# Performance work log

Measured on AMD Instinct MI355X. Metric: run time of the kernel, lower is better.

The kernel has to match this reference:

```python
import jax, jax.numpy as jnp
import numpy as np

NUM_ITER = 64
M_CONST = jnp.array([-1.0, 1.0], dtype=jnp.float32)      # constellation m
ALPHA   = jnp.array([0.5, 0.5], dtype=jnp.float32)       # prior alpha


def setup_inputs() -> dict:
    key = jax.random.key(0)
    k1, k2, k3 = jax.random.split(key, 3)
    B, N_RX, N_TX = 16384, 64, 32
    # channel matrix, scaled ~1/sqrt(N_rx) like a normalized MIMO channel
    Ht = jax.random.normal(k1, (B, N_RX, N_TX), dtype=jnp.float32) / jnp.sqrt(jnp.float32(N_RX))
    yt = jax.random.normal(k2, (B, N_RX), dtype=jnp.float32)
    sigmat0 = jax.random.uniform(k3, (B,), dtype=jnp.float32, minval=0.1, maxval=0.6)
    taui = jnp.ones((NUM_ITER + 1,), dtype=jnp.float32)          # taui0 = 1
    delta = jnp.full((NUM_ITER,), 0.01, dtype=jnp.float32)       # small step size for stability
    return {"yt": yt, "Ht": Ht, "sigmat0": sigmat0, "taui": taui, "delta": delta}


def _cmdnet(yt, Ht, sigmat0, taui, delta):
    m = M_CONST                      # [M]
    log_alpha = jnp.log(ALPHA)       # [M]
    sig2 = (sigmat0 ** 2)[:, None, None]          # [B,1,1]
    B, _, K = Ht.shape
    M = m.shape[0]

    # G0 = zeros broadcast to [B, K, M]
    G = jnp.zeros((B, K, M), dtype=Ht.dtype)
    tau = jnp.abs(taui[0])
    ft = jax.nn.softmax((log_alpha + G) * tau, axis=-1)   # [B,K,M]
    xt = jnp.sum(ft * m, axis=-1)                         # [B,K]

    HH = jnp.einsum('bnk,bnl->bkl', Ht, Ht)               # [B,K,K]
    yH = jnp.einsum('bn,bnk->bk', yt, Ht)                 # [B,K]

    def step(carry, xs):
        G, ft, xt, tau = carry
        d_i, tau_next = xs
        xHH = jnp.einsum('bk,bkl->bl', xt, HH)            # [B,K]
        grad_x = tau * (ft * m - ft * xt[..., None])      # [B,K,M]
        grad_L = sig2 * (1.0 - jnp.exp(-G)) + grad_x * (xHH - yH)[..., None]
        G = G - d_i * grad_L
        tau = jnp.abs(tau_next)
        ft = jax.nn.softmax((log_alpha + G) * tau, axis=-1)
        xt = jnp.sum(ft * m, axis=-1)
        return (G, ft, xt, tau), None

    (G, ft, xt, tau), _ = jax.lax.scan(step, (G, ft, xt, tau), (delta, taui[1:]))
    return ft, xt


def reference(yt, Ht, sigmat0, taui, delta):
    return _cmdnet(yt, Ht, sigmat0, taui, delta)
```

## Files before the change

kernel.cpp:

```cpp
#include <hip/hip_runtime.h>


#define NRX 64
#define KSYM 32

typedef float  f32x16 __attribute__((ext_vector_type(16)));
typedef short  short8 __attribute__((ext_vector_type(8)));

__device__ __forceinline__ float readlane_f(float v, int lane) {
    return __int_as_float(__builtin_amdgcn_readlane(__float_as_int(v), lane));
}
__device__ __forceinline__ unsigned cvt_pk_bf16(float a, float b) {
    unsigned r;
    asm("v_cvt_pk_bf16_f32 %0, %1, %2" : "=v"(r) : "v"(a), "v"(b));
    return r;
}

union FragU { unsigned u[4]; short8 s; };

__global__ __launch_bounds__(256, 8) void cmdnet_kernel(
    const float* __restrict__ yt,
    const float* __restrict__ Ht,
    const float* __restrict__ sigmat0,
    const float* __restrict__ taui,
    const float* __restrict__ delta,
    float* __restrict__ out_ft,
    float* __restrict__ out_xt,
    int niter)
{
    __shared__ __align__(16) float ytL[4][2][NRX];
    __shared__ __align__(16) float xtP[4][2][KSYM];

    const int tid  = threadIdx.x;
    const int w    = tid >> 6;
    const int lane = tid & 63;
    const int k    = lane & 31;
    const int h    = lane >> 5;
    const int hi8  = h * 8;
    const int bb   = blockIdx.x * 8 + w * 2;
    const int b    = bb + h;

    ytL[w][0][lane] = yt[(size_t)bb * NRX + lane];
    ytL[w][1][lane] = yt[(size_t)bb * NRX + NRX + lane];

    float dreg = 0.f, treg = 1.f;
    if (lane < niter) { dreg = delta[lane]; treg = fabsf(taui[lane + 1]); }

    float sig2 = sigmat0[b];
    sig2 *= sig2;

    f32x16 acc0, acc1;
    #pragma unroll
    for (int j = 0; j < 16; ++j) { acc0[j] = 0.f; acc1[j] = 0.f; }
    float yhp0 = 0.f, yhp1 = 0.f;

    #pragma unroll
    for (int s = 0; s < 2; ++s) {
        const float* Hb = Ht + ((size_t)(bb + s)) * (NRX * KSYM);
        #pragma unroll
        for (int c = 0; c < 4; ++c) {
            const float* base = Hb + (c * 16 + hi8) * KSYM + k;
            float f[8];
            #pragma unroll
            for (int e = 0; e < 8; ++e) f[e] = base[e * KSYM];

            float4 ya = *reinterpret_cast<const float4*>(&ytL[w][s][c * 16 + hi8]);
            float4 yb = *reinterpret_cast<const float4*>(&ytL[w][s][c * 16 + hi8 + 4]);
            float yp = (s == 0) ? yhp0 : yhp1;
            yp = fmaf(ya.x, f[0], yp); yp = fmaf(ya.y, f[1], yp);
            yp = fmaf(ya.z, f[2], yp); yp = fmaf(ya.w, f[3], yp);
            yp = fmaf(yb.x, f[4], yp); yp = fmaf(yb.y, f[5], yp);
            yp = fmaf(yb.z, f[6], yp); yp = fmaf(yb.w, f[7], yp);
            if (s == 0) yhp0 = yp; else yhp1 = yp;

            FragU hiF, loF;
            #pragma unroll
            for (int p = 0; p < 4; ++p) {
                unsigned hp = cvt_pk_bf16(f[2*p], f[2*p+1]);
                float h0 = __uint_as_float(hp << 16);
                float h1 = __uint_as_float(hp & 0xffff0000u);
                float l0 = f[2*p]   - h0;
                float l1 = f[2*p+1] - h1;
                hiF.u[p] = hp;
                loF.u[p] = cvt_pk_bf16(l0, l1);
            }
            if (s == 0) {
                acc0 = __builtin_amdgcn_mfma_f32_32x32x16_bf16(hiF.s, hiF.s, acc0, 0, 0, 0);
                acc0 = __builtin_amdgcn_mfma_f32_32x32x16_bf16(hiF.s, loF.s, acc0, 0, 0, 0);
                acc0 = __builtin_amdgcn_mfma_f32_32x32x16_bf16(loF.s, hiF.s, acc0, 0, 0, 0);
            } else {
                acc1 = __builtin_amdgcn_mfma_f32_32x32x16_bf16(hiF.s, hiF.s, acc1, 0, 0, 0);
                acc1 = __builtin_amdgcn_mfma_f32_32x32x16_bf16(hiF.s, loF.s, acc1, 0, 0, 0);
                acc1 = __builtin_amdgcn_mfma_f32_32x32x16_bf16(loF.s, hiF.s, acc1, 0, 0, 0);
            }
        }
    }

    float yh0 = yhp0 + __shfl_xor(yhp0, 32, 64);
    float yh1 = yhp1 + __shfl_xor(yhp1, 32, 64);
    float yh  = h ? yh1 : yh0;

    float own[16], oth[16];
    #pragma unroll
    for (int j = 0; j < 16; ++j) {
        float t = h ? acc1[j] : acc0[j];
        float u = h ? acc0[j] : acc1[j];
        own[j] = t;
        oth[j] = __shfl_xor(u, 32, 64);
    }

    float tau = fabsf(taui[0]);
    float G0 = 0.f, G1 = 0.f;
    float ft0 = 0.5f, ft1 = 0.5f, xt = 0.f;

    const int pos = ((k >> 2) & 1) * 16 + (k & 3) + ((k >> 3) << 2);
    const float4* xo = reinterpret_cast<const float4*>(&xtP[w][h][h * 16]);
    const float4* xx = reinterpret_cast<const float4*>(&xtP[w][h][(1 ^ h) * 16]);

    for (int i = 0; i < niter; ++i) {
        xtP[w][h][pos] = xt;

        float d        = readlane_f(dreg, i);
        float tau_next = readlane_f(treg, i);

        float a0 = -yh, a1 = 0.f, a2 = 0.f, a3 = 0.f;
        #pragma unroll
        for (int t = 0; t < 4; ++t) {
            float4 xa = xo[t];
            float4 xb = xx[t];
            a0 = fmaf(own[4*t+0], xa.x, a0);
            a1 = fmaf(own[4*t+1], xa.y, a1);
            a2 = fmaf(own[4*t+2], xa.z, a2);
            a3 = fmaf(own[4*t+3], xa.w, a3);
            a0 = fmaf(oth[4*t+0], xb.x, a0);
            a1 = fmaf(oth[4*t+1], xb.y, a1);
            a2 = fmaf(oth[4*t+2], xb.z, a2);
            a3 = fmaf(oth[4*t+3], xb.w, a3);
        }
        float r = (a0 + a1) + (a2 + a3);

        float p  = 2.f * tau * ft0 * ft1 * r;
        float e0 = __expf(-G0);
        float e1 = __expf(-G1);
        float g0 = fmaf(sig2, 1.f - e0, -p);
        float g1 = fmaf(sig2, 1.f - e1,  p);
        G0 = fmaf(-d, g0, G0);
        G1 = fmaf(-d, g1, G1);

        tau = tau_next;
        float z  = tau * (G1 - G0);
        float ez = __expf(-fabsf(z));
        float sg = __builtin_amdgcn_rcpf(1.f + ez);
        float abig = sg, asml = ez * sg;
        bool ps = (z >= 0.f);
        ft1 = ps ? abig : asml;
        ft0 = ps ? asml : abig;
        xt  = ft1 - ft0;
    }

    float2 f2 = make_float2(ft0, ft1);
    reinterpret_cast<float2*>(out_ft)[(size_t)b * KSYM + k] = f2;
    out_xt[(size_t)b * KSYM + k] = xt;
}

extern "C" void kernel_launch(void* const* d_in, const int* in_sizes, int n_in,
                              void* d_out, int out_size, void* d_ws, size_t ws_size,
                              hipStream_t stream) {
    const float* yt    = (const float*)d_in[0];
    const float* Ht    = (const float*)d_in[1];
    const float* sg    = (const float*)d_in[2];
    const float* taui  = (const float*)d_in[3];
    const float* delta = (const float*)d_in[4];
    int B     = in_sizes[2];
    int niter = in_sizes[4];
    float* out    = (float*)d_out;
    float* out_ft = out;
    float* out_xt = out + (size_t)B * 64;

    dim3 grid(B / 8), block(256);
    hipLaunchKernelGGL(cmdnet_kernel, grid, block, 0, stream,
                       yt, Ht, sg, taui, delta, out_ft, out_xt, niter);
}
```

Baseline: 90.31 us.

## Replace per-iteration LDS xt exchange with DPP row-rotation matvec

The HH accumulators are staged once through a new per-wave LDS buffer and regathered into a rotated diagonal order, so each lane holds the HH entries matching DPP row_ror shifts of xt. Inside the 64-iteration loop, the LDS store and float4 reads of xt are replaced by a single cross-half shuffle plus 30 DPP rotations feeding FMAs. This targets LDS latency and the write-read dependency on the serial critical path. In exchange it adds a 16 KB LDS buffer and more registers, and the launch-bounds occupancy hint drops from 8 to 4 blocks per CU.

```diff
diff --git a/kernel.cpp b/kernel.cpp
--- a/kernel.cpp
+++ b/kernel.cpp
@@ -15,10 +15,19 @@
     asm("v_cvt_pk_bf16_f32 %0, %1, %2" : "=v"(r) : "v"(a), "v"(b));
     return r;
 }
+template <int N>
+__device__ __forceinline__ float dpp_ror_f(float v) {
+    return __int_as_float(__builtin_amdgcn_update_dpp(
+        0, __float_as_int(v), 0x120 + N, 0xF, 0xF, true));
+}
+template <int N>
+__device__ __forceinline__ int dpp_ror_i(int v) {
+    return __builtin_amdgcn_update_dpp(0, v, 0x120 + N, 0xF, 0xF, true);
+}
 
 union FragU { unsigned u[4]; short8 s; };
 
-__global__ __launch_bounds__(256, 8) void cmdnet_kernel(
+__global__ __launch_bounds__(256, 4) void cmdnet_kernel(
     const float* __restrict__ yt,
     const float* __restrict__ Ht,
     const float* __restrict__ sigmat0,
@@ -28,8 +37,8 @@
     float* __restrict__ out_xt,
     int niter)
 {
+    __shared__ __align__(16) float hhbuf[4][KSYM * KSYM];
     __shared__ __align__(16) float ytL[4][2][NRX];
-    __shared__ __align__(16) float xtP[4][2][KSYM];
 
     const int tid  = threadIdx.x;
     const int w    = tid >> 6;
@@ -79,10 +88,8 @@
                 unsigned hp = cvt_pk_bf16(f[2*p], f[2*p+1]);
                 float h0 = __uint_as_float(hp << 16);
                 float h1 = __uint_as_float(hp & 0xffff0000u);
-                float l0 = f[2*p]   - h0;
-                float l1 = f[2*p+1] - h1;
+                loF.u[p] = cvt_pk_bf16(f[2*p] - h0, f[2*p+1] - h1);
                 hiF.u[p] = hp;
-                loF.u[p] = cvt_pk_bf16(l0, l1);
             }
             if (s == 0) {
                 acc0 = __builtin_amdgcn_mfma_f32_32x32x16_bf16(hiF.s, hiF.s, acc0, 0, 0, 0);
@@ -100,44 +107,54 @@
     float yh1 = yhp1 + __shfl_xor(yhp1, 32, 64);
     float yh  = h ? yh1 : yh0;
 
-    float own[16], oth[16];
+    float own_d[32];
+    const int low4 = k & 15;
+    float* buf = &hhbuf[w][0];
     #pragma unroll
-    for (int j = 0; j < 16; ++j) {
-        float t = h ? acc1[j] : acc0[j];
-        float u = h ? acc0[j] : acc1[j];
-        own[j] = t;
-        oth[j] = __shfl_xor(u, 32, 64);
+    for (int s = 0; s < 2; ++s) {
+        #pragma unroll
+        for (int j = 0; j < 16; ++j) {
+            int row = (j & 3) + 8 * (j >> 2) + 4 * h;
+            buf[row * 32 + k] = s ? acc1[j] : acc0[j];
+        }
+        if (h == s) {
+            const float* rowp = buf + k * 32;
+            own_d[0]  = rowp[k];
+            own_d[16] = rowp[k ^ 16];
+            #define GATH(J) { \
+                int idx = dpp_ror_i<J>(low4); \
+                own_d[J]        = rowp[(k & 16) | idx]; \
+                own_d[16 + (J)] = rowp[((k & 16) ^ 16) | idx]; }
+            GATH(1)  GATH(2)  GATH(3)  GATH(4)  GATH(5)
+            GATH(6)  GATH(7)  GATH(8)  GATH(9)  GATH(10)
+            GATH(11) GATH(12) GATH(13) GATH(14) GATH(15)
+            #undef GATH
+        }
     }
 
     float tau = fabsf(taui[0]);
     float G0 = 0.f, G1 = 0.f;
     float ft0 = 0.5f, ft1 = 0.5f, xt = 0.f;
 
-    const int pos = ((k >> 2) & 1) * 16 + (k & 3) + ((k >> 3) << 2);
-    const float4* xo = reinterpret_cast<const float4*>(&xtP[w][h][h * 16]);
-    const float4* xx = reinterpret_cast<const float4*>(&xtP[w][h][(1 ^ h) * 16]);
-
     for (int i = 0; i < niter; ++i) {
-        xtP[w][h][pos] = xt;
-
         float d        = readlane_f(dreg, i);
         float tau_next = readlane_f(treg, i);
 
-        float a0 = -yh, a1 = 0.f, a2 = 0.f, a3 = 0.f;
-        #pragma unroll
-        for (int t = 0; t < 4; ++t) {
-            float4 xa = xo[t];
-            float4 xb = xx[t];
-            a0 = fmaf(own[4*t+0], xa.x, a0);
-            a1 = fmaf(own[4*t+1], xa.y, a1);
-            a2 = fmaf(own[4*t+2], xa.z, a2);
-            a3 = fmaf(own[4*t+3], xa.w, a3);
-            a0 = fmaf(oth[4*t+0], xb.x, a0);
-            a1 = fmaf(oth[4*t+1], xb.y, a1);
-            a2 = fmaf(oth[4*t+2], xb.z, a2);
-            a3 = fmaf(oth[4*t+3], xb.w, a3);
-        }
-        float r = (a0 + a1) + (a2 + a3);
+        float xts = __shfl_xor(xt, 16, 64);
+        float a[4];
+        a[0] = fmaf(own_d[0], xt, -yh);
+        a[1] = own_d[16] * xts;
+        a[2] = 0.f; a[3] = 0.f;
+        #define STEP(J) { \
+            float ra = dpp_ror_f<J>(xt); \
+            float rb = dpp_ror_f<J>(xts); \
+            a[(J) & 3]       = fmaf(own_d[J],        ra, a[(J) & 3]); \
+            a[((J) + 2) & 3] = fmaf(own_d[16 + (J)], rb, a[((J) + 2) & 3]); }
+        STEP(1)  STEP(2)  STEP(3)  STEP(4)  STEP(5)
+        STEP(6)  STEP(7)  STEP(8)  STEP(9)  STEP(10)
+        STEP(11) STEP(12) STEP(13) STEP(14) STEP(15)
+        #undef STEP
+        float r = (a[0] + a[1]) + (a[2] + a[3]);
 
         float p  = 2.f * tau * ft0 * ft1 * r;
         float e0 = __expf(-G0);
```

Measured after the change: 87.74 us. -2.8%, faster.
